# Performance work log

Measured on AMD Instinct MI355X. Metric: run time of the kernel, lower is better.

The kernel has to match this reference:

```python
import jax, jax.numpy as jnp
import numpy as np

ENC_DIM = 1024
NUM_HEADS = 16
HEAD_DIM = ENC_DIM // NUM_HEADS
D_FF = 4 * ENC_DIM
EPS = 1e-5


def _layernorm(x, g, b):
    mu = jnp.mean(x, axis=-1, keepdims=True)
    var = jnp.mean((x - mu) ** 2, axis=-1, keepdims=True)
    return (x - mu) * jax.lax.rsqrt(var + EPS) * g + b


def setup_inputs() -> dict:
    key = jax.random.key(0)
    ks = jax.random.split(key, 12)
    s = 1.0 / np.sqrt(ENC_DIM)
    sf = 1.0 / np.sqrt(D_FF)
    x = jax.random.normal(ks[0], (2, 2048, ENC_DIM), dtype=jnp.float32)
    return {
        "x": x,
        "ln1_g": jnp.ones((ENC_DIM,), jnp.float32),
        "ln1_b": jnp.zeros((ENC_DIM,), jnp.float32),
        "wq": jax.random.uniform(ks[1], (ENC_DIM, ENC_DIM), jnp.float32, -s, s),
        "bq": jax.random.uniform(ks[2], (ENC_DIM,), jnp.float32, -s, s),
        "wk": jax.random.uniform(ks[3], (ENC_DIM, ENC_DIM), jnp.float32, -s, s),
        "bk": jax.random.uniform(ks[4], (ENC_DIM,), jnp.float32, -s, s),
        "wv": jax.random.uniform(ks[5], (ENC_DIM, ENC_DIM), jnp.float32, -s, s),
        "bv": jax.random.uniform(ks[6], (ENC_DIM,), jnp.float32, -s, s),
        "wo": jax.random.uniform(ks[7], (ENC_DIM, ENC_DIM), jnp.float32, -s, s),
        "bo": jax.random.uniform(ks[8], (ENC_DIM,), jnp.float32, -s, s),
        "w1": jax.random.uniform(ks[9], (ENC_DIM, D_FF), jnp.float32, -s, s),
        "b1": jax.random.uniform(ks[10], (D_FF,), jnp.float32, -s, s),
        "w2": jax.random.uniform(ks[11], (D_FF, ENC_DIM), jnp.float32, -sf, sf),
        "b2": jnp.zeros((ENC_DIM,), jnp.float32),
        "ln2_g": jnp.ones((ENC_DIM,), jnp.float32),
        "ln2_b": jnp.zeros((ENC_DIM,), jnp.float32),
    }


def reference(x, ln1_g, ln1_b, wq, bq, wk, bk, wv, bv, wo, bo, w1, b1, w2, b2, ln2_g, ln2_b):
    B, S, D = x.shape
    h = _layernorm(x, ln1_g, ln1_b)
    # QKV projections -> (B, H, S, hd)
    def split_heads(t):
        return t.reshape(B, S, NUM_HEADS, HEAD_DIM).transpose(0, 2, 1, 3)
    q = split_heads(h @ wq + bq)
    k = split_heads(h @ wk + bk)
    v = split_heads(h @ wv + bv)
    scores = jnp.einsum("bhqd,bhkd->bhqk", q, k) / np.sqrt(HEAD_DIM)
    probs = jax.nn.softmax(scores, axis=-1)
    attn = jnp.einsum("bhqk,bhkd->bhqd", probs, v)
    attn = attn.transpose(0, 2, 1, 3).reshape(B, S, D)
    x = attn @ wo + bo + x  # residual 1
    h2 = _layernorm(x, ln2_g, ln2_b)
    mlp = jax.nn.gelu(h2 @ w1 + b1, approximate=False) @ w2 + b2
    return x + mlp
```

## Files before the change

### kernel.cpp

```cpp
#include <hip/hip_runtime.h>

typedef unsigned short u16;
typedef unsigned int u32;
typedef __bf16 bf16x8 __attribute__((ext_vector_type(8)));
typedef float floatx4 __attribute__((ext_vector_type(4)));

__device__ __forceinline__ u16 f2bf(float f) {
    u32 u = __float_as_uint(f);
    u = (u + 0x7FFFu + ((u >> 16) & 1u)) >> 16;
    return (u16)u;
}

__device__ __forceinline__ void gld_lds16(const u16* g, u16* l) {
    __builtin_amdgcn_global_load_lds(
        (const __attribute__((address_space(1))) u32*)g,
        (__attribute__((address_space(3))) u32*)l, 16, 0, 0);
}

__device__ __forceinline__ float gelu_exact(float v) {
    const float z = fabsf(v) * 0.70710678118f;
    const float t = __builtin_amdgcn_rcpf(1.0f + 0.3275911f * z);
    const float e = __builtin_amdgcn_exp2f(-z * z * 1.44269504f);
    float poly = 1.061405429f;
    poly = poly * t - 1.453152027f;
    poly = poly * t + 1.421413741f;
    poly = poly * t - 0.284496736f;
    poly = poly * t + 0.254829592f;
    float erfz = 1.0f - poly * t * e;
    erfz = copysignf(erfz, v);
    return 0.5f * v * (1.0f + erfz);
}

__global__ __launch_bounds__(256) void transpose_cvt4(
    const float* __restrict__ s0, const float* __restrict__ s1,
    const float* __restrict__ s2, const float* __restrict__ s3,
    u16* __restrict__ d0, u16* __restrict__ d1,
    u16* __restrict__ d2, u16* __restrict__ d3)
{
    __shared__ float t[32][33];
    const int z = blockIdx.z;
    const float* src = z == 0 ? s0 : (z == 1 ? s1 : (z == 2 ? s2 : s3));
    u16* dst = z == 0 ? d0 : (z == 1 ? d1 : (z == 2 ? d2 : d3));
    const int bm = blockIdx.x * 32, bk = blockIdx.y * 32;
    const int tx = threadIdx.x & 31, ty = threadIdx.x >> 5;
    #pragma unroll
    for (int i = ty; i < 32; i += 8)
        t[i][tx] = src[(long)(bk + i) * 1024 + bm + tx];
    __syncthreads();
    #pragma unroll
    for (int i = ty; i < 32; i += 8)
        dst[(long)(bm + i) * 1024 + bk + tx] = f2bf(t[tx][i]);
}

__global__ __launch_bounds__(256) void transpose_cvt(
    const float* __restrict__ src, u16* __restrict__ dst, int K, int M)
{
    __shared__ float t[32][33];
    const int bm = blockIdx.x * 32, bk = blockIdx.y * 32;
    const int tx = threadIdx.x & 31, ty = threadIdx.x >> 5;
    #pragma unroll
    for (int i = ty; i < 32; i += 8)
        t[i][tx] = src[(long)(bk + i) * M + bm + tx];
    __syncthreads();
    #pragma unroll
    for (int i = ty; i < 32; i += 8)
        dst[(long)(bm + i) * K + bk + tx] = f2bf(t[tx][i]);
}

__global__ __launch_bounds__(256) void ln_kernel(
    const float* __restrict__ x, const float* __restrict__ g,
    const float* __restrict__ bta, u16* __restrict__ out)
{
    const int row = blockIdx.x;
    const int tid = threadIdx.x;
    const float4 v = ((const float4*)(x + (long)row * 1024))[tid];
    float s  = v.x + v.y + v.z + v.w;
    float s2 = v.x*v.x + v.y*v.y + v.z*v.z + v.w*v.w;
    #pragma unroll
    for (int off = 1; off < 64; off <<= 1) {
        s  += __shfl_xor(s, off);
        s2 += __shfl_xor(s2, off);
    }
    __shared__ float red[8];
    const int wave = tid >> 6, lane = tid & 63;
    if (lane == 0) { red[wave] = s; red[4 + wave] = s2; }
    __syncthreads();
    s  = red[0] + red[1] + red[2] + red[3];
    s2 = red[4] + red[5] + red[6] + red[7];
    const float mu   = s * (1.0f / 1024.0f);
    const float var  = s2 * (1.0f / 1024.0f) - mu * mu;
    const float rstd = rsqrtf(var + 1e-5f);
    const int c = tid << 2;
    ushort4 o;
    o.x = f2bf((v.x - mu) * rstd * g[c + 0] + bta[c + 0]);
    o.y = f2bf((v.y - mu) * rstd * g[c + 1] + bta[c + 1]);
    o.z = f2bf((v.z - mu) * rstd * g[c + 2] + bta[c + 2]);
    o.w = f2bf((v.w - mu) * rstd * g[c + 3] + bta[c + 3]);
    ((ushort4*)(out + (long)row * 1024))[tid] = o;
}

__global__ __launch_bounds__(256) void combine2_kernel(
    float* __restrict__ out, const float* __restrict__ p1,
    const float* __restrict__ res, const float* __restrict__ bias, int mmask)
{
    const int t = blockIdx.x * 256 + threadIdx.x;
    const float4 a = ((const float4*)out)[t];
    const float4 c = ((const float4*)p1)[t];
    const float4 r = ((const float4*)res)[t];
    const float4 b = ((const float4*)bias)[t & mmask];
    float4 o;
    o.x = a.x + c.x + r.x + b.x;
    o.y = a.y + c.y + r.y + b.y;
    o.z = a.z + c.z + r.z + b.z;
    o.w = a.w + c.w + r.w + b.w;
    ((float4*)out)[t] = o;
}

__global__ __launch_bounds__(256) void vtrans_kernel(
    const u16* __restrict__ V, u16* __restrict__ Vt)
{
    __shared__ u16 t[64][72];
    const int bh = blockIdx.y, s0 = blockIdx.x << 6;
    const int tid = threadIdx.x;
    const long base = (long)bh * 2048 * 64;
    const int row = tid >> 2, seg = tid & 3;
    *(uint4*)&t[row][seg << 3] =
        *(const uint4*)(V + base + (long)(s0 + row) * 64 + (seg << 3));
    *(uint4*)&t[row][(seg + 4) << 3] =
        *(const uint4*)(V + base + (long)(s0 + row) * 64 + ((seg + 4) << 3));
    __syncthreads();
    #pragma unroll
    for (int half = 0; half < 2; ++half) {
        const int sl = (seg + (half << 2)) << 3;
        u16 tmp[8];
        #pragma unroll
        for (int j = 0; j < 8; ++j) tmp[j] = t[sl + j][row];
        *(uint4*)(Vt + base + (long)row * 2048 + s0 + sl) = *(uint4*)tmp;
    }
}

template<int MODE, int BN>
__global__ __launch_bounds__(256) void gemm_kernel(
    const u16* __restrict__ A, const u16* __restrict__ Bt,
    const float* __restrict__ bias0, const float* __restrict__ bias1,
    const float* __restrict__ bias2, const float* __restrict__ res,
    float* __restrict__ part1, void* __restrict__ outv, int K, int M)
{
    constexpr int MS  = (BN == 128) ? 4 : 2;
    constexpr int NIB = (BN == 128) ? 4 : 2;
    __shared__ u16 As[128 * 64];
    __shared__ u16 Bs[BN * 64];
    const int tid = threadIdx.x, lane = tid & 63, wave = tid >> 6;
    const int wm = (BN == 128) ? ((wave >> 1) << 6) : (wave << 5);
    const int wn = (BN == 128) ? ((wave & 1) << 6) : 0;
    const int lrow = lane & 15, quad = lane >> 4;
    const int sl = lrow & 7;
    const long rowbase = (long)blockIdx.y * 128;
    const long colbase = (long)blockIdx.x * BN;
    int kstart = 0, kend = K;
    if constexpr (MODE == 3) {
        kstart = blockIdx.z * (K >> 1);
        kend   = kstart + (K >> 1);
    }

    const u16* gA[4]; int lA[4];
    #pragma unroll
    for (int i = 0; i < 4; ++i) {
        const int cid = (i << 6) + lane;
        const int rl = cid >> 3, p = cid & 7, q = p ^ (rl & 7);
        gA[i] = A + (rowbase + (wave << 5) + rl) * (long)K + kstart + (q << 3);
        lA[i] = ((wave << 5) + rl) * 64 + (p << 3);
    }
    const u16* gB[NIB]; int lB[NIB];
    #pragma unroll
    for (int i = 0; i < NIB; ++i) {
        const int cid = (i << 6) + lane;
        const int rl = cid >> 3, p = cid & 7, q = p ^ (rl & 7);
        const int rw = (BN == 128) ? (wave << 5) : (wave << 4);
        gB[i] = Bt + (colbase + rw + rl) * (long)K + kstart + (q << 3);
        lB[i] = (rw + rl) * 64 + (p << 3);
    }

    floatx4 acc[MS][4];
    #pragma unroll
    for (int i = 0; i < MS; ++i)
        #pragma unroll
        for (int j = 0; j < 4; ++j)
            acc[i][j] = floatx4{0.f, 0.f, 0.f, 0.f};

    for (int k0 = kstart; k0 < kend; k0 += 64) {
        __syncthreads();
        #pragma unroll
        for (int i = 0; i < 4; ++i) { gld_lds16(gA[i], As + lA[i]); gA[i] += 64; }
        #pragma unroll
        for (int i = 0; i < NIB; ++i) { gld_lds16(gB[i], Bs + lB[i]); gB[i] += 64; }
        __syncthreads();
        #pragma unroll
        for (int kc = 0; kc < 2; ++kc) {
            const int ph = (((kc << 2) + quad) ^ sl) << 3;
            bf16x8 af[MS], bf[4];
            #pragma unroll
            for (int ms = 0; ms < MS; ++ms)
                af[ms] = *(const bf16x8*)&As[(wm + (ms << 4) + lrow) * 64 + ph];
            #pragma unroll
            for (int ns = 0; ns < 4; ++ns)
                bf[ns] = *(const bf16x8*)&Bs[(wn + (ns << 4) + lrow) * 64 + ph];
            #pragma unroll
            for (int ms = 0; ms < MS; ++ms)
                #pragma unroll
                for (int ns = 0; ns < 4; ++ns)
                    acc[ms][ns] = __builtin_amdgcn_mfma_f32_16x16x32_bf16(
                        af[ms], bf[ns], acc[ms][ns], 0, 0, 0);
        }
    }

    float* tgt = nullptr;
    if constexpr (MODE == 3) tgt = blockIdx.z ? part1 : (float*)outv;
    #pragma unroll
    for (int ms = 0; ms < MS; ++ms) {
        #pragma unroll
        for (int ns = 0; ns < 4; ++ns) {
            const long col = colbase + wn + (ns << 4) + lrow;
            float bv = 0.f;
            if constexpr (MODE == 0) {
                const int which = (int)(col >> 10);
                const float* bp = which == 0 ? bias0 : (which == 1 ? bias1 : bias2);
                bv = bp[col & 1023];
            } else if constexpr (MODE == 1 || MODE == 2) {
                bv = bias0[col];
            }
            #pragma unroll
            for (int r = 0; r < 4; ++r) {
                const long row = rowbase + wm + (ms << 4) + (quad << 2) + r;
                float v = acc[ms][ns][r] + bv;
                if constexpr (MODE == 0) {
                    const long which = col >> 10;
                    if (which == 0) v *= 0.18033688f;
                    const long b = row >> 11, s = row & 2047;
                    const long h = (col >> 6) & 15, d = col & 63;
                    ((u16*)outv)[which * 4194304 + (((b << 4) + h) * 2048 + s) * 64 + d] = f2bf(v);
                } else if constexpr (MODE == 1) {
                    const long idx = row * M + col;
                    ((float*)outv)[idx] = v + res[idx];
                } else if constexpr (MODE == 2) {
                    ((u16*)outv)[row * M + col] = f2bf(gelu_exact(v));
                } else {
                    tgt[row * M + col] = v;
                }
            }
        }
    }
}

__global__ __launch_bounds__(256) void attn_kernel(
    const u16* __restrict__ Q, const u16* __restrict__ Kp,
    const u16* __restrict__ Vt, u16* __restrict__ O)
{
    __shared__ u16 Ks[2][4096];
    __shared__ u16 Vs[2][4096];
    __shared__ u16 Ps[4][2][16][72];
    const int tid = threadIdx.x, lane = tid & 63, wave = tid >> 6;
    const int lrow = lane & 15, quad = lane >> 4;
    const int bh = blockIdx.y;
    const long kvbase = (long)bh * 2048 * 64;
    const int qbase = (blockIdx.x << 7) + (wave << 5);

    const int srow = lane >> 3;
    const int schunk = (lane & 7) ^ srow;
    const int i0 = wave << 1;
    const u16* kg0 = Kp + kvbase + (long)(((i0 << 3) + srow) * 64 + (schunk << 3));
    const u16* kg1 = kg0 + 8 * 64;
    const u16* vg0 = Vt + kvbase + (long)(((i0 << 3) + srow) * 2048 + (schunk << 3));
    const u16* vg1 = vg0 + 8 * 2048;
    const int lofs = i0 << 9;

    bf16x8 qf[2][2];
    #pragma unroll
    for (int g = 0; g < 2; ++g)
        #pragma unroll
        for (int h = 0; h < 2; ++h)
            qf[g][h] = *(const bf16x8*)(Q + kvbase +
                (long)(qbase + (g << 4) + lrow) * 64 + (quad << 3) + (h << 5));

    int aoff[4][2];
    #pragma unroll
    for (int ns = 0; ns < 4; ++ns)
        #pragma unroll
        for (int h = 0; h < 2; ++h)
            aoff[ns][h] = ((ns << 4) + lrow) * 64 +
                          (((quad + (h << 2)) ^ (lrow & 7)) << 3);

    floatx4 oacc[2][4];
    #pragma unroll
    for (int g = 0; g < 2; ++g)
        #pragma unroll
        for (int ns = 0; ns < 4; ++ns)
            oacc[g][ns] = floatx4{0.f, 0.f, 0.f, 0.f};
    float lr[2] = {0.f, 0.f};

    gld_lds16(kg0, &Ks[0][lofs]);
    gld_lds16(kg1, &Ks[0][lofs + 512]);
    gld_lds16(vg0, &Vs[0][lofs]);
    gld_lds16(vg1, &Vs[0][lofs + 512]);
    kg0 += 4096; kg1 += 4096;
    int vofs = 64;

    for (int it = 0; it < 32; ++it) {
        const int cur = it & 1;
        __syncthreads();
        if (it < 31) {
            const int nxt = cur ^ 1;
            gld_lds16(kg0, &Ks[nxt][lofs]);
            gld_lds16(kg1, &Ks[nxt][lofs + 512]);
            gld_lds16(vg0 + vofs, &Vs[nxt][lofs]);
            gld_lds16(vg1 + vofs, &Vs[nxt][lofs + 512]);
            kg0 += 4096; kg1 += 4096; vofs += 64;
        }
        const u16* ks = &Ks[cur][0];
        const u16* vs = &Vs[cur][0];

        floatx4 st[2][4];
        #pragma unroll
        for (int ns = 0; ns < 4; ++ns) {
            const bf16x8 af0 = *(const bf16x8*)&ks[aoff[ns][0]];
            const bf16x8 af1 = *(const bf16x8*)&ks[aoff[ns][1]];
            floatx4 z = floatx4{0.f, 0.f, 0.f, 0.f};
            st[0][ns] = __builtin_amdgcn_mfma_f32_16x16x32_bf16(af0, qf[0][0], z, 0, 0, 0);
            st[0][ns] = __builtin_amdgcn_mfma_f32_16x16x32_bf16(af1, qf[0][1], st[0][ns], 0, 0, 0);
            st[1][ns] = __builtin_amdgcn_mfma_f32_16x16x32_bf16(af0, qf[1][0], z, 0, 0, 0);
            st[1][ns] = __builtin_amdgcn_mfma_f32_16x16x32_bf16(af1, qf[1][1], st[1][ns], 0, 0, 0);
        }

        bf16x8 pf[2][2];
        #pragma unroll
        for (int g = 0; g < 2; ++g) {
            float rs = 0.f;
            #pragma unroll
            for (int ns = 0; ns < 4; ++ns) {
                const float p0 = __builtin_amdgcn_exp2f(st[g][ns][0]);
                const float p1 = __builtin_amdgcn_exp2f(st[g][ns][1]);
                const float p2 = __builtin_amdgcn_exp2f(st[g][ns][2]);
                const float p3 = __builtin_amdgcn_exp2f(st[g][ns][3]);
                rs += (p0 + p1) + (p2 + p3);
                uint2 w;
                w.x = __builtin_amdgcn_perm(__float_as_uint(p1) + 0x8000u,
                                            __float_as_uint(p0) + 0x8000u, 0x07060302u);
                w.y = __builtin_amdgcn_perm(__float_as_uint(p3) + 0x8000u,
                                            __float_as_uint(p2) + 0x8000u, 0x07060302u);
                *(uint2*)&Ps[wave][g][lrow][(ns << 4) + (quad << 2)] = w;
            }
            rs += __shfl_xor(rs, 16);
            rs += __shfl_xor(rs, 32);
            lr[g] += rs;
            pf[g][0] = *(const bf16x8*)&Ps[wave][g][lrow][quad << 3];
            pf[g][1] = *(const bf16x8*)&Ps[wave][g][lrow][(quad << 3) + 32];
        }

        #pragma unroll
        for (int ns = 0; ns < 4; ++ns) {
            const bf16x8 vf0 = *(const bf16x8*)&vs[aoff[ns][0]];
            const bf16x8 vf1 = *(const bf16x8*)&vs[aoff[ns][1]];
            #pragma unroll
            for (int g = 0; g < 2; ++g) {
                oacc[g][ns] = __builtin_amdgcn_mfma_f32_16x16x32_bf16(
                    pf[g][0], vf0, oacc[g][ns], 0, 0, 0);
                oacc[g][ns] = __builtin_amdgcn_mfma_f32_16x16x32_bf16(
                    pf[g][1], vf1, oacc[g][ns], 0, 0, 0);
            }
        }
    }

    const int b = bh >> 4, h = bh & 15;
    #pragma unroll
    for (int g = 0; g < 2; ++g) {
        float linv[4];
        #pragma unroll
        for (int r = 0; r < 4; ++r)
            linv[r] = 1.0f / __shfl(lr[g], (quad << 2) + r);
        #pragma unroll
        for (int ns = 0; ns < 4; ++ns)
            #pragma unroll
            for (int r = 0; r < 4; ++r) {
                const int q = qbase + (g << 4) + (quad << 2) + r;
                const long token = (long)b * 2048 + q;
                O[token * 1024 + (h << 6) + (ns << 4) + lrow] =
                    f2bf(oacc[g][ns][r] * linv[r]);
            }
    }
}

extern "C" void kernel_launch(void* const* d_in, const int* in_sizes, int n_in,
                              void* d_out, int out_size, void* d_ws, size_t ws_size,
                              hipStream_t stream)
{
    const float* x     = (const float*)d_in[0];
    const float* ln1_g = (const float*)d_in[1];
    const float* ln1_b = (const float*)d_in[2];
    const float* wq    = (const float*)d_in[3];
    const float* bq    = (const float*)d_in[4];
    const float* wk    = (const float*)d_in[5];
    const float* bk    = (const float*)d_in[6];
    const float* wv    = (const float*)d_in[7];
    const float* bv    = (const float*)d_in[8];
    const float* wo    = (const float*)d_in[9];
    const float* bo    = (const float*)d_in[10];
    const float* w1    = (const float*)d_in[11];
    const float* b1    = (const float*)d_in[12];
    const float* w2    = (const float*)d_in[13];
    const float* b2    = (const float*)d_in[14];
    const float* ln2_g = (const float*)d_in[15];
    const float* ln2_b = (const float*)d_in[16];
    float* out = (float*)d_out;

    char* w = (char*)d_ws;
    const size_t MB = 1024 * 1024;
    u16*   wqkvt = (u16*)(w + 0);
    u16*   wot   = (u16*)(w + 6  * MB);
    u16*   w1t   = (u16*)(w + 8  * MB);
    u16*   w2t   = (u16*)(w + 16 * MB);
    u16*   h1    = (u16*)(w + 24 * MB);
    u16*   qkvb  = (u16*)(w + 32 * MB);
    u16*   vtb   = (u16*)(w + 56 * MB);
    float* x1    = (float*)(w + 64 * MB);
    float* part1 = (float*)(w + 80 * MB);
    u16*   ffb   = (u16*)(w + 32 * MB);
    u16*   qb = qkvb;
    u16*   kb = qkvb + 4194304;
    u16*   vb = qkvb + 8388608;

    transpose_cvt4<<<dim3(32, 32, 4), 256, 0, stream>>>(
        wq, wk, wv, wo, wqkvt, wqkvt + 1048576, wqkvt + 2097152, wot);
    transpose_cvt<<<dim3(128, 32), 256, 0, stream>>>(w1, w1t, 1024, 4096);
    transpose_cvt<<<dim3(32, 128), 256, 0, stream>>>(w2, w2t, 4096, 1024);

    ln_kernel<<<4096, 256, 0, stream>>>(x, ln1_g, ln1_b, h1);

    gemm_kernel<0, 128><<<dim3(24, 32), 256, 0, stream>>>(
        h1, wqkvt, bq, bk, bv, nullptr, nullptr, qkvb, 1024, 3072);

    vtrans_kernel<<<dim3(32, 32), 256, 0, stream>>>(vb, vtb);

    attn_kernel<<<dim3(16, 32), 256, 0, stream>>>(qb, kb, vtb, h1);

    gemm_kernel<1, 64><<<dim3(16, 32), 256, 0, stream>>>(
        h1, wot, bo, nullptr, nullptr, x, nullptr, x1, 1024, 1024);

    ln_kernel<<<4096, 256, 0, stream>>>(x1, ln2_g, ln2_b, h1);

    gemm_kernel<2, 128><<<dim3(32, 32), 256, 0, stream>>>(
        h1, w1t, b1, nullptr, nullptr, nullptr, nullptr, ffb, 1024, 4096);

    gemm_kernel<3, 64><<<dim3(16, 32, 2), 256, 0, stream>>>(
        ffb, w2t, nullptr, nullptr, nullptr, nullptr, part1, out, 4096, 1024);

    combine2_kernel<<<4096, 256, 0, stream>>>(out, part1, x1, b2, 255);
}
```

Baseline: 387.2 us.

## Double-buffer GEMM LDS tiles with 32-wide K steps to overlap loads

Splits the GEMM shared-memory tiles into two K=32 buffers and prefetches the next K slice into the alternate buffer while MFMAs run on the current one. This leaves one barrier per iteration and is meant to hide global-to-LDS load latency behind compute. The XOR swizzle is reworked for the 32-wide rows. The cost is that the K step is halved, so there are twice as many barriers and loop iterations with less MFMA work between them.

```diff
diff --git a/kernel.cpp b/kernel.cpp
--- a/kernel.cpp
+++ b/kernel.cpp
@@ -147,14 +147,13 @@
     float* __restrict__ part1, void* __restrict__ outv, int K, int M)
 {
     constexpr int MS  = (BN == 128) ? 4 : 2;
-    constexpr int NIB = (BN == 128) ? 4 : 2;
-    __shared__ u16 As[128 * 64];
-    __shared__ u16 Bs[BN * 64];
+    constexpr int NIB = (BN == 128) ? 2 : 1;
+    __shared__ u16 As[2][128 * 32];
+    __shared__ u16 Bs[2][BN * 32];
     const int tid = threadIdx.x, lane = tid & 63, wave = tid >> 6;
     const int wm = (BN == 128) ? ((wave >> 1) << 6) : (wave << 5);
     const int wn = (BN == 128) ? ((wave & 1) << 6) : 0;
     const int lrow = lane & 15, quad = lane >> 4;
-    const int sl = lrow & 7;
     const long rowbase = (long)blockIdx.y * 128;
     const long colbase = (long)blockIdx.x * BN;
     int kstart = 0, kend = K;
@@ -163,23 +162,24 @@
         kend   = kstart + (K >> 1);
     }
 
-    const u16* gA[4]; int lA[4];
-    #pragma unroll
-    for (int i = 0; i < 4; ++i) {
-        const int cid = (i << 6) + lane;
-        const int rl = cid >> 3, p = cid & 7, q = p ^ (rl & 7);
-        gA[i] = A + (rowbase + (wave << 5) + rl) * (long)K + kstart + (q << 3);
-        lA[i] = ((wave << 5) + rl) * 64 + (p << 3);
+    const u16* gA[2]; int lA[2];
+    #pragma unroll
+    for (int i = 0; i < 2; ++i) {
+        const int cid = (i << 8) + tid;
+        const int rl = cid >> 2, p = cid & 3, q = p ^ ((rl >> 1) & 3);
+        gA[i] = A + (rowbase + rl) * (long)K + kstart + (q << 3);
+        lA[i] = cid << 3;
     }
     const u16* gB[NIB]; int lB[NIB];
     #pragma unroll
     for (int i = 0; i < NIB; ++i) {
-        const int cid = (i << 6) + lane;
-        const int rl = cid >> 3, p = cid & 7, q = p ^ (rl & 7);
-        const int rw = (BN == 128) ? (wave << 5) : (wave << 4);
-        gB[i] = Bt + (colbase + rw + rl) * (long)K + kstart + (q << 3);
-        lB[i] = (rw + rl) * 64 + (p << 3);
-    }
+        const int cid = (i << 8) + tid;
+        const int rl = cid >> 2, p = cid & 3, q = p ^ ((rl >> 1) & 3);
+        gB[i] = Bt + (colbase + rl) * (long)K + kstart + (q << 3);
+        lB[i] = cid << 3;
+    }
+
+    const int ph = (quad ^ ((lrow >> 1) & 3)) << 3;
 
     floatx4 acc[MS][4];
     #pragma unroll
@@ -188,30 +188,36 @@
         for (int j = 0; j < 4; ++j)
             acc[i][j] = floatx4{0.f, 0.f, 0.f, 0.f};
 
-    for (int k0 = kstart; k0 < kend; k0 += 64) {
+    const int nIt = (kend - kstart) >> 5;
+
+    #pragma unroll
+    for (int i = 0; i < 2; ++i) { gld_lds16(gA[i], &As[0][lA[i]]); gA[i] += 32; }
+    #pragma unroll
+    for (int i = 0; i < NIB; ++i) { gld_lds16(gB[i], &Bs[0][lB[i]]); gB[i] += 32; }
+
+    for (int it = 0; it < nIt; ++it) {
+        const int cur = it & 1;
         __syncthreads();
-        #pragma unroll
-        for (int i = 0; i < 4; ++i) { gld_lds16(gA[i], As + lA[i]); gA[i] += 64; }
-        #pragma unroll
-        for (int i = 0; i < NIB; ++i) { gld_lds16(gB[i], Bs + lB[i]); gB[i] += 64; }
-        __syncthreads();
-        #pragma unroll
-        for (int kc = 0; kc < 2; ++kc) {
-            const int ph = (((kc << 2) + quad) ^ sl) << 3;
-            bf16x8 af[MS], bf[4];
-            #pragma unroll
-            for (int ms = 0; ms < MS; ++ms)
-                af[ms] = *(const bf16x8*)&As[(wm + (ms << 4) + lrow) * 64 + ph];
+        if (it + 1 < nIt) {
+            const int nxt = cur ^ 1;
+            #pragma unroll
+            for (int i = 0; i < 2; ++i) { gld_lds16(gA[i], &As[nxt][lA[i]]); gA[i] += 32; }
+            #pragma unroll
+            for (int i = 0; i < NIB; ++i) { gld_lds16(gB[i], &Bs[nxt][lB[i]]); gB[i] += 32; }
+        }
+        bf16x8 af[MS], bf[4];
+        #pragma unroll
+        for (int ms = 0; ms < MS; ++ms)
+            af[ms] = *(const bf16x8*)&As[cur][(wm + (ms << 4) + lrow) * 32 + ph];
+        #pragma unroll
+        for (int ns = 0; ns < 4; ++ns)
+            bf[ns] = *(const bf16x8*)&Bs[cur][(wn + (ns << 4) + lrow) * 32 + ph];
+        #pragma unroll
+        for (int ms = 0; ms < MS; ++ms)
             #pragma unroll
             for (int ns = 0; ns < 4; ++ns)
-                bf[ns] = *(const bf16x8*)&Bs[(wn + (ns << 4) + lrow) * 64 + ph];
-            #pragma unroll
-            for (int ms = 0; ms < MS; ++ms)
-                #pragma unroll
-                for (int ns = 0; ns < 4; ++ns)
-                    acc[ms][ns] = __builtin_amdgcn_mfma_f32_16x16x32_bf16(
-                        af[ms], bf[ns], acc[ms][ns], 0, 0, 0);
-        }
+                acc[ms][ns] = __builtin_amdgcn_mfma_f32_16x16x32_bf16(
+                    af[ms], bf[ns], acc[ms][ns], 0, 0, 0);
     }
 
     float* tgt = nullptr;
```

After: 394.6 us. Within noise of the previous version (+1.9%).
